# Kernel tuning notes

Hardware: AMD Instinct MI355X
Metric: run time of the kernel (lower is better)

The kernel has to match this reference:

```python
import jax, jax.numpy as jnp
import numpy as np

B, C_IN, H, W = 16, 3, 512, 512
C_OUT = 16
K = 15  # kernel_size; effective kernel is [C_OUT, C_IN, 1, K]


def setup_inputs() -> dict:
    key = jax.random.key(0)
    x = jax.random.normal(key, (B, C_IN, H, W), dtype=jnp.float32)
    scale = jnp.ones((), dtype=jnp.float32)  # nn.Parameter s=1.0
    return {"x": x, "scale": scale}


def reference(x, scale):
    # create_kernel: parabolic structuring element w[n] = -z_n^2 / (4*scale)
    # z = linspace(-K//2 + 1, K//2, K)  (python: (-K)//2 + 1 = -7 for K=15)
    z = jnp.linspace((-K) // 2 + 1, K // 2, K, dtype=jnp.float32)
    w = -(z ** 2) / (4.0 * scale)  # [K]

    half = K // 2  # M=1 so no vertical padding
    xp = jnp.pad(x, ((0, 0), (0, 0), (0, 0), (half, half)),
                 constant_values=-jnp.inf)  # aggregation identity

    # Max-plus conv: out = max over (c_in, tap) of x_pad[..., w+n] + w[n].
    # Loop over K taps (small fixed kernel dim) -> [B, C_in, H, W, K]
    shifted = jnp.stack([xp[..., n:n + W] + w[n] for n in range(K)], axis=-1)
    base = jnp.max(shifted, axis=(1, 4))  # [B, H, W]

    # Kernel is identical for every (c_out, c_in) pair (repeat), so all
    # output channels are equal: broadcast to [B, C_out, H, W].
    return jnp.broadcast_to(base[:, None, :, :], (B, C_OUT, H, W))
```

## Files before the change

kernel.cpp:

```cpp
#include <hip/hip_runtime.h>
#include <math.h>


#define BB   16
#define CIN  3
#define HH   512
#define WW   512
#define COUT 16
#define KK   15
#define HALF 7
#define ROWS 4
#define TPB  256

typedef float floatx4 __attribute__((ext_vector_type(4)));


__global__ __launch_bounds__(TPB) void semiconv_kernel(
    const float* __restrict__ x, const float* __restrict__ scale_p,
    float* __restrict__ out)
{
    __shared__ __align__(16) float m[ROWS][528];
    const int t  = threadIdx.x;
    const int wv = t >> 6;
    const int i  = t & 63;
    const int g  = blockIdx.x;
    const int b  = g >> 7;
    const int h  = ((g & 127) << 2) + wv;

    const float inv4s = 0.25f / scale_p[0];

    const float*  xrow = x + ((size_t)(b * CIN) * HH + h) * (size_t)WW;
    const size_t  cs   = (size_t)HH * WW;
    {
        const float* p0 = xrow + 4 * i;
        floatx4 a0 = *(const floatx4*)(p0);
        floatx4 b0 = *(const floatx4*)(p0 + 256);
        floatx4 a1 = *(const floatx4*)(p0 + cs);
        floatx4 b1 = *(const floatx4*)(p0 + cs + 256);
        floatx4 a2 = *(const floatx4*)(p0 + 2 * cs);
        floatx4 b2 = *(const floatx4*)(p0 + 2 * cs + 256);
        floatx4 s0, s1;
        s0.x = fmaxf(fmaxf(a0.x, a1.x), a2.x);
        s0.y = fmaxf(fmaxf(a0.y, a1.y), a2.y);
        s0.z = fmaxf(fmaxf(a0.z, a1.z), a2.z);
        s0.w = fmaxf(fmaxf(a0.w, a1.w), a2.w);
        s1.x = fmaxf(fmaxf(b0.x, b1.x), b2.x);
        s1.y = fmaxf(fmaxf(b0.y, b1.y), b2.y);
        s1.z = fmaxf(fmaxf(b0.z, b1.z), b2.z);
        s1.w = fmaxf(fmaxf(b0.w, b1.w), b2.w);
        *(floatx4*)&m[wv][8 + 4 * i]       = s0;
        *(floatx4*)&m[wv][8 + 256 + 4 * i] = s1;
    }
    {
        const floatx4 ninf = {-INFINITY, -INFINITY, -INFINITY, -INFINITY};
        if (i < 2)       *(floatx4*)&m[wv][4 * i]              = ninf;
        else if (i > 61) *(floatx4*)&m[wv][520 + 4 * (i - 62)] = ninf;
    }
    asm volatile("s_waitcnt lgkmcnt(0)" ::: "memory");

    float wt[KK];
    #pragma unroll
    for (int n = 0; n < KK; ++n) {
        float z = (float)(n - HALF);
        wt[n] = -(z * z) * inv4s;
    }

    floatx4 rv[2];
    #pragma unroll
    for (int s = 0; s < 2; ++s) {
        const int w0 = s * 256 + 4 * i;
        float v[20];
        #pragma unroll
        for (int k = 0; k < 5; ++k) {
            floatx4 a = *(const floatx4*)&m[wv][w0 + 4 * k];
            v[4 * k + 0] = a.x; v[4 * k + 1] = a.y;
            v[4 * k + 2] = a.z; v[4 * k + 3] = a.w;
        }
        float res[4];
        #pragma unroll
        for (int j = 0; j < 4; ++j) {
            float best = v[j + 1] + wt[0];
            #pragma unroll
            for (int n = 1; n < KK; ++n)
                best = fmaxf(best, v[j + n + 1] + wt[n]);
            res[j] = best;
        }
        rv[s].x = res[0]; rv[s].y = res[1]; rv[s].z = res[2]; rv[s].w = res[3];
    }

    float* ob = out + ((size_t)(b * COUT) * HH + h) * (size_t)WW + 4 * i;
    #pragma unroll
    for (int c = 0; c < COUT; ++c) {
        float* p = ob + (size_t)c * cs;
        __builtin_nontemporal_store(rv[0], (floatx4*)p);
        __builtin_nontemporal_store(rv[1], (floatx4*)(p + 256));
    }
}

extern "C" void kernel_launch(void* const* d_in, const int* in_sizes, int n_in,
                              void* d_out, int out_size, void* d_ws, size_t ws_size,
                              hipStream_t stream) {
    const float* x     = (const float*)d_in[0];
    const float* scale = (const float*)d_in[1];
    float* out         = (float*)d_out;

    dim3 grid(BB * HH / ROWS);
    dim3 block(TPB);
    hipLaunchKernelGGL(semiconv_kernel, grid, block, 0, stream, x, scale, out);
}
```

Baseline: 56.77 us.

## Split into base compute kernel plus separate broadcast copy kernel

Computes the single max-plus base plane into a workspace buffer, then runs a second kernel that copies it to all 16 output channels with contiguous per-plane streaming writes instead of 16 strided nontemporal stores per thread. The goal is more sequential write patterns in the dominant 256MB-scale output. It adds an extra launch plus a read and write of the base buffer, and drops the nontemporal stores.

Result: slower. 68.63 us (+20.9%).

```diff
diff --git a/kernel.cpp b/kernel.cpp
--- a/kernel.cpp
+++ b/kernel.cpp
@@ -15,9 +15,9 @@
 typedef float floatx4 __attribute__((ext_vector_type(4)));
 
 
-__global__ __launch_bounds__(TPB) void semiconv_kernel(
+__global__ __launch_bounds__(TPB) void semiconv_base_kernel(
     const float* __restrict__ x, const float* __restrict__ scale_p,
-    float* __restrict__ out)
+    float* __restrict__ base)
 {
     __shared__ __align__(16) float m[ROWS][528];
     const int t  = threadIdx.x;
@@ -29,8 +29,8 @@
 
     const float inv4s = 0.25f / scale_p[0];
 
-    const float*  xrow = x + ((size_t)(b * CIN) * HH + h) * (size_t)WW;
-    const size_t  cs   = (size_t)HH * WW;
+    const float* xrow = x + ((size_t)(b * CIN) * HH + h) * (size_t)WW;
+    const size_t cs   = (size_t)HH * WW;
     {
         const float* p0 = xrow + 4 * i;
         floatx4 a0 = *(const floatx4*)(p0);
@@ -65,7 +65,7 @@
         wt[n] = -(z * z) * inv4s;
     }
 
-    floatx4 rv[2];
+    float* orow = base + ((size_t)b * HH + h) * (size_t)WW + 4 * i;
     #pragma unroll
     for (int s = 0; s < 2; ++s) {
         const int w0 = s * 256 + 4 * i;
@@ -85,15 +85,28 @@
                 best = fmaxf(best, v[j + n + 1] + wt[n]);
             res[j] = best;
         }
-        rv[s].x = res[0]; rv[s].y = res[1]; rv[s].z = res[2]; rv[s].w = res[3];
+        floatx4 rv;
+        rv.x = res[0]; rv.y = res[1]; rv.z = res[2]; rv.w = res[3];
+        *(floatx4*)(orow + s * 256) = rv;
     }
+}
 
-    float* ob = out + ((size_t)(b * COUT) * HH + h) * (size_t)WW + 4 * i;
-    #pragma unroll
-    for (int c = 0; c < COUT; ++c) {
-        float* p = ob + (size_t)c * cs;
-        __builtin_nontemporal_store(rv[0], (floatx4*)p);
-        __builtin_nontemporal_store(rv[1], (floatx4*)(p + 256));
+
+__global__ __launch_bounds__(TPB) void broadcast_kernel(
+    const float* __restrict__ base, float* __restrict__ out)
+{
+    const int t        = threadIdx.x;
+    const int blk      = blockIdx.x;
+    const int plane_id = blk >> 3;
+    const int sub      = blk & 7;
+    const int b        = plane_id >> 4;
+
+    const floatx4* src = (const floatx4*)base + ((size_t)b << 16) + (sub << 13) + t;
+    floatx4*       dst = (floatx4*)out + ((size_t)plane_id << 16) + (sub << 13) + t;
+
+    #pragma unroll 8
+    for (int k = 0; k < 32; ++k) {
+        dst[k * 256] = src[k * 256];
     }
 }
 
@@ -103,8 +116,10 @@
     const float* x     = (const float*)d_in[0];
     const float* scale = (const float*)d_in[1];
     float* out         = (float*)d_out;
+    float* base        = (float*)d_ws;
 
-    dim3 grid(BB * HH / ROWS);
-    dim3 block(TPB);
-    hipLaunchKernelGGL(semiconv_kernel, grid, block, 0, stream, x, scale, out);
+    hipLaunchKernelGGL(semiconv_base_kernel, dim3(BB * HH / ROWS), dim3(TPB),
+                       0, stream, x, scale, base);
+    hipLaunchKernelGGL(broadcast_kernel, dim3(BB * COUT * 8), dim3(TPB),
+                       0, stream, base, out);
 }
```
